# Optimization experiments

Hardware: AMD Instinct MI355X
Metric: run time of the kernel (lower is better)

## Reference

```python
import jax, jax.numpy as jnp
import numpy as np


def _mdca_one_exit(cam, target):
    # cam: [B, C, H, W] -> adaptive_avg_pool2d(cam, 1).squeeze() == mean over H, W
    logits = cam.mean(axis=(2, 3))            # [B, C]
    B, C = logits.shape
    avg_conf = logits.mean(axis=0)            # [C] per-class mean logit
    counts = jnp.bincount(target, length=C)   # [C] label histogram
    avg_count = counts.astype(logits.dtype) / jnp.asarray(B, logits.dtype)
    return jnp.mean(jnp.abs(avg_conf - avg_count))  # sum/C == mean


def setup_inputs() -> dict:
    key = jax.random.key(0)
    ks = jax.random.split(key, 5)
    B, C, H, W = 128, 1000, 14, 14
    inp = {}
    for i in range(4):
        inp[f'cam_{i}'] = jax.random.normal(ks[i], (B, C, H, W), dtype=jnp.float32)
    inp['target'] = jax.random.randint(ks[4], (B,), 0, C, dtype=jnp.int64)
    return inp


def reference(cam_0, cam_1, cam_2, cam_3, target):
    cams = (cam_0, cam_1, cam_2, cam_3)
    return tuple(_mdca_one_exit(c, target) for c in cams)
```

## Files before the change

### kernel.cpp

```cpp
#include <hip/hip_runtime.h>
#include <hip/hip_bf16.h>


constexpr int B  = 128;
constexpr int C  = 1000;
constexpr int HW = 196;
constexpr int HW4 = HW / 4;

__global__ __launch_bounds__(256) void class_sum_kernel(
    const float* __restrict__ c0, const float* __restrict__ c1,
    const float* __restrict__ c2, const float* __restrict__ c3,
    float* __restrict__ sums)
{
    const int c   = blockIdx.x;
    const int cam = blockIdx.y;
    const float* __restrict__ src =
        (cam == 0) ? c0 : (cam == 1) ? c1 : (cam == 2) ? c2 : c3;

    float acc = 0.0f;
    const int total4 = B * HW4;
    for (int i = threadIdx.x; i < total4; i += 256) {
        const int b = i / HW4;
        const int j = i - b * HW4;
        const float4 v = *reinterpret_cast<const float4*>(
            src + (size_t)(b * C + c) * HW + (size_t)j * 4);
        acc += (v.x + v.y) + (v.z + v.w);
    }

    #pragma unroll
    for (int off = 32; off > 0; off >>= 1)
        acc += __shfl_down(acc, off, 64);

    __shared__ float red[4];
    const int wid  = threadIdx.x >> 6;
    const int lane = threadIdx.x & 63;
    if (lane == 0) red[wid] = acc;
    __syncthreads();
    if (threadIdx.x == 0) {
        float s = (red[0] + red[1]) + (red[2] + red[3]);
        sums[cam * C + c] = s;
    }
}

__global__ __launch_bounds__(1024) void finalize_kernel(
    const float* __restrict__ sums, const int* __restrict__ target,
    float* __restrict__ out)
{
    __shared__ int   cnt[C];
    __shared__ float red[16];

    const int cam = blockIdx.x;

    for (int c = threadIdx.x; c < C; c += 1024) cnt[c] = 0;
    __syncthreads();
    if (threadIdx.x < B) atomicAdd(&cnt[target[threadIdx.x]], 1);
    __syncthreads();

    const float inv_BHW = 1.0f / (float)(B * HW);
    const float inv_B   = 1.0f / (float)B;

    float acc = 0.0f;
    for (int c = threadIdx.x; c < C; c += 1024) {
        const float avg_conf  = sums[cam * C + c] * inv_BHW;
        const float avg_count = (float)cnt[c] * inv_B;
        acc += fabsf(avg_conf - avg_count);
    }

    #pragma unroll
    for (int off = 32; off > 0; off >>= 1)
        acc += __shfl_down(acc, off, 64);

    const int wid  = threadIdx.x >> 6;
    const int lane = threadIdx.x & 63;
    if (lane == 0) red[wid] = acc;
    __syncthreads();
    if (threadIdx.x == 0) {
        float s = 0.0f;
        #pragma unroll
        for (int w = 0; w < 16; ++w) s += red[w];
        out[cam] = s * (1.0f / (float)C);
    }
}

extern "C" void kernel_launch(void* const* d_in, const int* in_sizes, int n_in,
                              void* d_out, int out_size, void* d_ws, size_t ws_size,
                              hipStream_t stream) {
    const float* c0 = (const float*)d_in[0];
    const float* c1 = (const float*)d_in[1];
    const float* c2 = (const float*)d_in[2];
    const float* c3 = (const float*)d_in[3];
    const int*   target = (const int*)d_in[4];

    float* sums = (float*)d_ws;

    dim3 grid1(C, 4);
    class_sum_kernel<<<grid1, 256, 0, stream>>>(c0, c1, c2, c3, sums);
    finalize_kernel<<<4, 1024, 0, stream>>>(sums, target, (float*)d_out);
}
```

Measured before the change: 75.99 us.

## Restructure class reduction into per-thread row sums with three-stage reduction

Replaces the one-block-per-class reduction with a grid where each thread walks whole contiguous HW rows for one class across a slice of the batch. It writes 64 partial sums per class, which a second kernel combines with the label histogram into per-group absolute errors, and a third kernel combines those into the outputs. The aim is more independent memory streams per thread and less strided indexing arithmetic. In exchange, neighbouring lanes now read addresses 784 bytes apart, so each vector load is uncoalesced and depends on cache reuse across iterations. It also adds a kernel launch and an extra pass over the partial-sum buffer.

```diff
diff --git a/kernel.cpp b/kernel.cpp
--- a/kernel.cpp
+++ b/kernel.cpp
@@ -2,83 +2,88 @@
 #include <hip/hip_bf16.h>
 
 
-constexpr int B  = 128;
-constexpr int C  = 1000;
-constexpr int HW = 196;
-constexpr int HW4 = HW / 4;
+constexpr int B   = 128;
+constexpr int C   = 1000;
+constexpr int HW  = 196;
+constexpr int HW4 = 49;
 
-__global__ __launch_bounds__(256) void class_sum_kernel(
+constexpr int NS    = 64;
+constexpr int BPS   = B / NS;
+constexpr int CHUNK = 256;
+constexpr int NCH   = 4;
+
+constexpr int G   = 8;
+constexpr int CPG = C / G;
+
+__global__ __launch_bounds__(256) void stage1_kernel(
     const float* __restrict__ c0, const float* __restrict__ c1,
     const float* __restrict__ c2, const float* __restrict__ c3,
-    float* __restrict__ sums)
+    float* __restrict__ partial)
 {
-    const int c   = blockIdx.x;
-    const int cam = blockIdx.y;
+    const int c   = blockIdx.x * CHUNK + threadIdx.x;
+    const int s   = blockIdx.y;
+    const int cam = blockIdx.z;
     const float* __restrict__ src =
         (cam == 0) ? c0 : (cam == 1) ? c1 : (cam == 2) ? c2 : c3;
+    if (c >= C) return;
 
     float acc = 0.0f;
-    const int total4 = B * HW4;
-    for (int i = threadIdx.x; i < total4; i += 256) {
-        const int b = i / HW4;
-        const int j = i - b * HW4;
-        const float4 v = *reinterpret_cast<const float4*>(
-            src + (size_t)(b * C + c) * HW + (size_t)j * 4);
-        acc += (v.x + v.y) + (v.z + v.w);
+    for (int bb = 0; bb < BPS; ++bb) {
+        const int b = s * BPS + bb;
+        const float4* __restrict__ p =
+            reinterpret_cast<const float4*>(src) + (size_t)(b * C + c) * HW4;
+        #pragma unroll 7
+        for (int j = 0; j < HW4; ++j) {
+            const float4 v = p[j];
+            acc += (v.x + v.y) + (v.z + v.w);
+        }
+    }
+    partial[(cam * NS + s) * C + c] = acc;
+}
+
+__global__ __launch_bounds__(128) void stage2_kernel(
+    const float* __restrict__ partial, const int* __restrict__ target,
+    float* __restrict__ ws2)
+{
+    __shared__ int   cnt[C];
+    __shared__ float red[2];
+
+    const int cam = blockIdx.x >> 3;
+    const int g   = blockIdx.x & 7;
+    const int tid = threadIdx.x;
+
+    for (int i = tid; i < C; i += 128) cnt[i] = 0;
+    __syncthreads();
+    if (tid < B) atomicAdd(&cnt[target[tid]], 1);
+    __syncthreads();
+
+    float acc = 0.0f;
+    if (tid < CPG) {
+        const int c = g * CPG + tid;
+        float ssum = 0.0f;
+        #pragma unroll 8
+        for (int k = 0; k < NS; ++k)
+            ssum += partial[(cam * NS + k) * C + c];
+        acc = fabsf(ssum * (1.0f / (float)(B * HW))
+                    - (float)cnt[c] * (1.0f / (float)B));
     }
 
     #pragma unroll
     for (int off = 32; off > 0; off >>= 1)
         acc += __shfl_down(acc, off, 64);
-
-    __shared__ float red[4];
-    const int wid  = threadIdx.x >> 6;
-    const int lane = threadIdx.x & 63;
-    if (lane == 0) red[wid] = acc;
+    if ((tid & 63) == 0) red[tid >> 6] = acc;
     __syncthreads();
-    if (threadIdx.x == 0) {
-        float s = (red[0] + red[1]) + (red[2] + red[3]);
-        sums[cam * C + c] = s;
-    }
+    if (tid == 0) ws2[blockIdx.x] = red[0] + red[1];
 }
 
-__global__ __launch_bounds__(1024) void finalize_kernel(
-    const float* __restrict__ sums, const int* __restrict__ target,
-    float* __restrict__ out)
+__global__ void stage3_kernel(const float* __restrict__ ws2,
+                              float* __restrict__ out)
 {
-    __shared__ int   cnt[C];
-    __shared__ float red[16];
-
-    const int cam = blockIdx.x;
-
-    for (int c = threadIdx.x; c < C; c += 1024) cnt[c] = 0;
-    __syncthreads();
-    if (threadIdx.x < B) atomicAdd(&cnt[target[threadIdx.x]], 1);
-    __syncthreads();
-
-    const float inv_BHW = 1.0f / (float)(B * HW);
-    const float inv_B   = 1.0f / (float)B;
-
-    float acc = 0.0f;
-    for (int c = threadIdx.x; c < C; c += 1024) {
-        const float avg_conf  = sums[cam * C + c] * inv_BHW;
-        const float avg_count = (float)cnt[c] * inv_B;
-        acc += fabsf(avg_conf - avg_count);
-    }
-
-    #pragma unroll
-    for (int off = 32; off > 0; off >>= 1)
-        acc += __shfl_down(acc, off, 64);
-
-    const int wid  = threadIdx.x >> 6;
-    const int lane = threadIdx.x & 63;
-    if (lane == 0) red[wid] = acc;
-    __syncthreads();
-    if (threadIdx.x == 0) {
+    if (threadIdx.x < 4) {
         float s = 0.0f;
         #pragma unroll
-        for (int w = 0; w < 16; ++w) s += red[w];
-        out[cam] = s * (1.0f / (float)C);
+        for (int i = 0; i < G; ++i) s += ws2[threadIdx.x * G + i];
+        out[threadIdx.x] = s * (1.0f / (float)C);
     }
 }
 
@@ -91,9 +96,11 @@
     const float* c3 = (const float*)d_in[3];
     const int*   target = (const int*)d_in[4];
 
-    float* sums = (float*)d_ws;
+    float* partial = (float*)d_ws;
+    float* ws2     = (float*)((char*)d_ws + 1048576);
 
-    dim3 grid1(C, 4);
-    class_sum_kernel<<<grid1, 256, 0, stream>>>(c0, c1, c2, c3, sums);
-    finalize_kernel<<<4, 1024, 0, stream>>>(sums, target, (float*)d_out);
+    dim3 grid1(NCH, NS, 4);
+    stage1_kernel<<<grid1, 256, 0, stream>>>(c0, c1, c2, c3, partial);
+    stage2_kernel<<<32, 128, 0, stream>>>(partial, target, ws2);
+    stage3_kernel<<<1, 64, 0, stream>>>(ws2, (float*)d_out);
 }
```

Measured after the change: 102.5 us. 1.35x slower.
